# Performance work log

Hardware: AMD Instinct MI355X
Metric: run time of the kernel (lower is better)

## Reference

```python
import jax, jax.numpy as jnp
import numpy as np

F = 32          # field_size == len(feature_sizes) == mpl_dims[0]
V = 10000       # per-field vocab
D = 496         # embedding_size == comb(F, 2)
H = 1024        # mpl_dims[1]
OUT = 1         # mpl_dims[-1]
B = 16384


def setup_inputs() -> dict:
    key = jax.random.key(0)
    ks = jax.random.split(key, 8)
    xv = jax.random.normal(ks[0], (B, F), dtype=jnp.float32)
    xi = jax.random.randint(ks[1], (B, F), 0, V, dtype=jnp.int64)
    # stacked per-field embedding tables: [F, V, D]
    emb = jax.random.normal(ks[2], (F, V, D), dtype=jnp.float32) * 0.05
    W1 = jax.random.normal(ks[3], (F, H), dtype=jnp.float32) * (1.0 / np.sqrt(F))
    b1 = jax.random.normal(ks[4], (H,), dtype=jnp.float32) * 0.01
    W2 = jax.random.normal(ks[5], (H + D, OUT), dtype=jnp.float32) * (1.0 / np.sqrt(H + D))
    b2 = jax.random.normal(ks[6], (OUT,), dtype=jnp.float32) * 0.01
    return {"xv": xv, "xi": xi, "emb": emb, "W1": W1, "b1": b1, "W2": W2, "b2": b2}


def reference(xv, xi, emb, W1, b1, W2, b2):
    # Per-field embedding gather, scaled by the field value: e[b,f,:] = emb[f, xi[b,f], :] * xv[b,f]
    gathered = jax.vmap(lambda table, idx: table[idx], in_axes=(0, 1), out_axes=1)(emb, xi)  # [B, F, D]
    e = gathered * xv[:, :, None]
    # FM sum-square minus square-sum interaction -> [B, D]
    s = jnp.sum(e, axis=1)
    qi = 0.5 * (s * s - jnp.sum(e * e, axis=1))
    # MLP branch on raw values (dropout inactive at inference)
    h = jax.nn.relu(xv @ W1 + b1)  # [B, H]
    x = jnp.concatenate([qi, h], axis=1)  # [B, D + H]
    return x @ W2 + b2  # [B, OUT]
```

## Files before the change

### kernel.cpp

```cpp
#include <hip/hip_runtime.h>

constexpr int F  = 32;
constexpr int V  = 10000;
constexpr int D  = 496;
constexpr int H  = 1024;

__global__ __launch_bounds__(256, 6) void fm_kernel(
    const float* __restrict__ xv,
    const int*   __restrict__ xi,
    const float* __restrict__ emb,
    const float* __restrict__ W2,
    const float* __restrict__ b2,
    float* __restrict__ out,
    int B)
{
    const int t  = threadIdx.x;
    const int w  = t >> 6;
    const int l  = t & 63;
    const int b0 = blockIdx.x * 4;

    __shared__ float        s_xv[4][F];
    __shared__ const float* s_row[4][F];

    if (t < 128) {
        const int rr = t >> 5, f = t & 31;
        const int r  = min(b0 + rr, B - 1);
        s_xv[rr][f]  = xv[(size_t)r * F + f];
        s_row[rr][f] = emb + ((size_t)f * V + (size_t)xi[(size_t)r * F + f]) * D;
    }
    __syncthreads();

    const int   c1 = (l < 60) ? l : 59;
    const float m1 = (l < 60) ? 1.0f : 0.0f;

    float4 s0  = make_float4(0.f, 0.f, 0.f, 0.f);
    float4 ss0 = make_float4(0.f, 0.f, 0.f, 0.f);
    float4 s1  = make_float4(0.f, 0.f, 0.f, 0.f);
    float4 ss1 = make_float4(0.f, 0.f, 0.f, 0.f);

    #pragma unroll 4
    for (int f = 0; f < F; ++f) {
        const float  xf = s_xv[w][f];
        const float* p  = s_row[w][f];
        float4 v0 = *reinterpret_cast<const float4*>(p + 4 * l);
        float4 v1 = *reinterpret_cast<const float4*>(p + 256 + 4 * c1);
        v0.x *= xf; v0.y *= xf; v0.z *= xf; v0.w *= xf;
        v1.x *= xf; v1.y *= xf; v1.z *= xf; v1.w *= xf;
        s0.x  += v0.x;        s0.y  += v0.y;        s0.z  += v0.z;        s0.w  += v0.w;
        ss0.x += v0.x * v0.x; ss0.y += v0.y * v0.y; ss0.z += v0.z * v0.z; ss0.w += v0.w * v0.w;
        s1.x  += v1.x;        s1.y  += v1.y;        s1.z  += v1.z;        s1.w  += v1.w;
        ss1.x += v1.x * v1.x; ss1.y += v1.y * v1.y; ss1.z += v1.z * v1.z; ss1.w += v1.w * v1.w;
    }

    const float4 w2a = *reinterpret_cast<const float4*>(W2 + 4 * l);
    const float4 w2b = *reinterpret_cast<const float4*>(W2 + 256 + 4 * c1);

    float acc = (0.5f * (s0.x * s0.x - ss0.x)) * w2a.x
              + (0.5f * (s0.y * s0.y - ss0.y)) * w2a.y
              + (0.5f * (s0.z * s0.z - ss0.z)) * w2a.z
              + (0.5f * (s0.w * s0.w - ss0.w)) * w2a.w
        + m1 * ((0.5f * (s1.x * s1.x - ss1.x)) * w2b.x
              + (0.5f * (s1.y * s1.y - ss1.y)) * w2b.y
              + (0.5f * (s1.z * s1.z - ss1.z)) * w2b.z
              + (0.5f * (s1.w * s1.w - ss1.w)) * w2b.w);

    #pragma unroll
    for (int off = 32; off > 0; off >>= 1)
        acc += __shfl_down(acc, off, 64);
    if (l == 0 && b0 + w < B) out[b0 + w] = acc + b2[0];
}

constexpr int R  = 64;
constexpr int RC = 8;

__global__ __launch_bounds__(256, 4) void mlp_kernel(
    const float* __restrict__ xv,
    const float* __restrict__ W1,
    const float* __restrict__ b1,
    const float* __restrict__ W2,
    float* __restrict__ out,
    int B)
{
    const int t  = threadIdx.x;
    const int b0 = blockIdx.x * R;
    const int j0 = 4 * t;

    __shared__ float s_xv[F][R];
    __shared__ float s_red[RC][4];

    {
        const int r0 = t >> 3, f0 = 4 * (t & 7);
        const int rA = min(b0 + r0,      B - 1);
        const int rB = min(b0 + r0 + 32, B - 1);
        float4 v0 = *reinterpret_cast<const float4*>(xv + (size_t)rA * F + f0);
        float4 v1 = *reinterpret_cast<const float4*>(xv + (size_t)rB * F + f0);
        s_xv[f0 + 0][r0] = v0.x; s_xv[f0 + 1][r0] = v0.y;
        s_xv[f0 + 2][r0] = v0.z; s_xv[f0 + 3][r0] = v0.w;
        s_xv[f0 + 0][r0 + 32] = v1.x; s_xv[f0 + 1][r0 + 32] = v1.y;
        s_xv[f0 + 2][r0 + 32] = v1.z; s_xv[f0 + 3][r0 + 32] = v1.w;
    }
    __syncthreads();

    const float4 w2v = *reinterpret_cast<const float4*>(W2 + D + j0);
    const float4 bv  = *reinterpret_cast<const float4*>(b1 + j0);

    for (int rc = 0; rc < R; rc += RC) {
        float4 h[RC];
        #pragma unroll
        for (int r = 0; r < RC; ++r) h[r] = bv;

        #pragma unroll 4
        for (int f = 0; f < F; ++f) {
            const float4 w  = *reinterpret_cast<const float4*>(W1 + f * H + j0);
            const float4 xa = *reinterpret_cast<const float4*>(&s_xv[f][rc]);
            const float4 xb = *reinterpret_cast<const float4*>(&s_xv[f][rc + 4]);
            const float xr[RC] = {xa.x, xa.y, xa.z, xa.w, xb.x, xb.y, xb.z, xb.w};
            #pragma unroll
            for (int r = 0; r < RC; ++r) {
                h[r].x += xr[r] * w.x; h[r].y += xr[r] * w.y;
                h[r].z += xr[r] * w.z; h[r].w += xr[r] * w.w;
            }
        }

        #pragma unroll
        for (int r = 0; r < RC; ++r) {
            float p = fmaxf(h[r].x, 0.f) * w2v.x + fmaxf(h[r].y, 0.f) * w2v.y
                    + fmaxf(h[r].z, 0.f) * w2v.z + fmaxf(h[r].w, 0.f) * w2v.w;
            #pragma unroll
            for (int off = 32; off > 0; off >>= 1)
                p += __shfl_down(p, off, 64);
            if ((t & 63) == 0) s_red[r][t >> 6] = p;
        }
        __syncthreads();
        if (t < RC) {
            const int row = b0 + rc + t;
            if (row < B)
                out[row] += s_red[t][0] + s_red[t][1] + s_red[t][2] + s_red[t][3];
        }
        __syncthreads();
    }
}

extern "C" void kernel_launch(void* const* d_in, const int* in_sizes, int n_in,
                              void* d_out, int out_size, void* d_ws, size_t ws_size,
                              hipStream_t stream) {
    const float* xv  = (const float*)d_in[0];
    const int*   xi  = (const int*)d_in[1];
    const float* emb = (const float*)d_in[2];
    const float* W1  = (const float*)d_in[3];
    const float* b1  = (const float*)d_in[4];
    const float* W2  = (const float*)d_in[5];
    const float* b2  = (const float*)d_in[6];
    float* out = (float*)d_out;

    const int B = in_sizes[0] / F;

    fm_kernel<<<(B + 3) / 4, 256, 0, stream>>>(xv, xi, emb, W2, b2, out, B);
    mlp_kernel<<<(B + R - 1) / R, 256, 0, stream>>>(xv, W1, b1, W2, out, B);
}
```

Baseline: 899.3 us.

## Merge FM and MLP kernels into one heterogeneous launch with combine pass

Fuses the FM gather kernel and the MLP kernel into a single grid, where the first nMLP blocks run the MLP branch and the rest run the FM branch. Partial results go to workspace, and a small combine kernel sums them with the bias. The aim is to let the compute-heavy MLP blocks overlap with the memory-bound gather blocks instead of running them one after the other. The fused kernel uses the MLP's lower occupancy bound (256,4) for the FM path too, and the extra combine launch adds a little overhead.

New measurement: 838.6 us. 6.8% less time.

```diff
diff --git a/kernel.cpp b/kernel.cpp
--- a/kernel.cpp
+++ b/kernel.cpp
@@ -4,141 +4,142 @@
 constexpr int V  = 10000;
 constexpr int D  = 496;
 constexpr int H  = 1024;
+constexpr int RM = 64;
+constexpr int RC = 8;
 
-__global__ __launch_bounds__(256, 6) void fm_kernel(
+__global__ __launch_bounds__(256, 4) void deepqi_hetero(
     const float* __restrict__ xv,
     const int*   __restrict__ xi,
     const float* __restrict__ emb,
-    const float* __restrict__ W2,
-    const float* __restrict__ b2,
-    float* __restrict__ out,
-    int B)
-{
-    const int t  = threadIdx.x;
-    const int w  = t >> 6;
-    const int l  = t & 63;
-    const int b0 = blockIdx.x * 4;
-
-    __shared__ float        s_xv[4][F];
-    __shared__ const float* s_row[4][F];
-
-    if (t < 128) {
-        const int rr = t >> 5, f = t & 31;
-        const int r  = min(b0 + rr, B - 1);
-        s_xv[rr][f]  = xv[(size_t)r * F + f];
-        s_row[rr][f] = emb + ((size_t)f * V + (size_t)xi[(size_t)r * F + f]) * D;
-    }
-    __syncthreads();
-
-    const int   c1 = (l < 60) ? l : 59;
-    const float m1 = (l < 60) ? 1.0f : 0.0f;
-
-    float4 s0  = make_float4(0.f, 0.f, 0.f, 0.f);
-    float4 ss0 = make_float4(0.f, 0.f, 0.f, 0.f);
-    float4 s1  = make_float4(0.f, 0.f, 0.f, 0.f);
-    float4 ss1 = make_float4(0.f, 0.f, 0.f, 0.f);
-
-    #pragma unroll 4
-    for (int f = 0; f < F; ++f) {
-        const float  xf = s_xv[w][f];
-        const float* p  = s_row[w][f];
-        float4 v0 = *reinterpret_cast<const float4*>(p + 4 * l);
-        float4 v1 = *reinterpret_cast<const float4*>(p + 256 + 4 * c1);
-        v0.x *= xf; v0.y *= xf; v0.z *= xf; v0.w *= xf;
-        v1.x *= xf; v1.y *= xf; v1.z *= xf; v1.w *= xf;
-        s0.x  += v0.x;        s0.y  += v0.y;        s0.z  += v0.z;        s0.w  += v0.w;
-        ss0.x += v0.x * v0.x; ss0.y += v0.y * v0.y; ss0.z += v0.z * v0.z; ss0.w += v0.w * v0.w;
-        s1.x  += v1.x;        s1.y  += v1.y;        s1.z  += v1.z;        s1.w  += v1.w;
-        ss1.x += v1.x * v1.x; ss1.y += v1.y * v1.y; ss1.z += v1.z * v1.z; ss1.w += v1.w * v1.w;
-    }
-
-    const float4 w2a = *reinterpret_cast<const float4*>(W2 + 4 * l);
-    const float4 w2b = *reinterpret_cast<const float4*>(W2 + 256 + 4 * c1);
-
-    float acc = (0.5f * (s0.x * s0.x - ss0.x)) * w2a.x
-              + (0.5f * (s0.y * s0.y - ss0.y)) * w2a.y
-              + (0.5f * (s0.z * s0.z - ss0.z)) * w2a.z
-              + (0.5f * (s0.w * s0.w - ss0.w)) * w2a.w
-        + m1 * ((0.5f * (s1.x * s1.x - ss1.x)) * w2b.x
-              + (0.5f * (s1.y * s1.y - ss1.y)) * w2b.y
-              + (0.5f * (s1.z * s1.z - ss1.z)) * w2b.z
-              + (0.5f * (s1.w * s1.w - ss1.w)) * w2b.w);
-
-    #pragma unroll
-    for (int off = 32; off > 0; off >>= 1)
-        acc += __shfl_down(acc, off, 64);
-    if (l == 0 && b0 + w < B) out[b0 + w] = acc + b2[0];
-}
-
-constexpr int R  = 64;
-constexpr int RC = 8;
-
-__global__ __launch_bounds__(256, 4) void mlp_kernel(
-    const float* __restrict__ xv,
     const float* __restrict__ W1,
     const float* __restrict__ b1,
     const float* __restrict__ W2,
-    float* __restrict__ out,
-    int B)
+    float* __restrict__ ws,
+    int B, int nMLP)
 {
-    const int t  = threadIdx.x;
-    const int b0 = blockIdx.x * R;
-    const int j0 = 4 * t;
+    const int t = threadIdx.x;
 
-    __shared__ float s_xv[F][R];
-    __shared__ float s_red[RC][4];
+    if ((int)blockIdx.x < nMLP) {
+        const int b0 = blockIdx.x * RM;
+        const int j0 = 4 * t;
 
-    {
-        const int r0 = t >> 3, f0 = 4 * (t & 7);
-        const int rA = min(b0 + r0,      B - 1);
-        const int rB = min(b0 + r0 + 32, B - 1);
-        float4 v0 = *reinterpret_cast<const float4*>(xv + (size_t)rA * F + f0);
-        float4 v1 = *reinterpret_cast<const float4*>(xv + (size_t)rB * F + f0);
-        s_xv[f0 + 0][r0] = v0.x; s_xv[f0 + 1][r0] = v0.y;
-        s_xv[f0 + 2][r0] = v0.z; s_xv[f0 + 3][r0] = v0.w;
-        s_xv[f0 + 0][r0 + 32] = v1.x; s_xv[f0 + 1][r0 + 32] = v1.y;
-        s_xv[f0 + 2][r0 + 32] = v1.z; s_xv[f0 + 3][r0 + 32] = v1.w;
-    }
-    __syncthreads();
+        __shared__ float s_xv[F][RM];
+        __shared__ float s_red[RC][4];
 
-    const float4 w2v = *reinterpret_cast<const float4*>(W2 + D + j0);
-    const float4 bv  = *reinterpret_cast<const float4*>(b1 + j0);
+        {
+            const int r0 = t >> 3, f0 = 4 * (t & 7);
+            const int rA = min(b0 + r0,      B - 1);
+            const int rB = min(b0 + r0 + 32, B - 1);
+            float4 v0 = *reinterpret_cast<const float4*>(xv + (size_t)rA * F + f0);
+            float4 v1 = *reinterpret_cast<const float4*>(xv + (size_t)rB * F + f0);
+            s_xv[f0 + 0][r0] = v0.x; s_xv[f0 + 1][r0] = v0.y;
+            s_xv[f0 + 2][r0] = v0.z; s_xv[f0 + 3][r0] = v0.w;
+            s_xv[f0 + 0][r0 + 32] = v1.x; s_xv[f0 + 1][r0 + 32] = v1.y;
+            s_xv[f0 + 2][r0 + 32] = v1.z; s_xv[f0 + 3][r0 + 32] = v1.w;
+        }
+        __syncthreads();
 
-    for (int rc = 0; rc < R; rc += RC) {
-        float4 h[RC];
-        #pragma unroll
-        for (int r = 0; r < RC; ++r) h[r] = bv;
+        const float4 w2v = *reinterpret_cast<const float4*>(W2 + D + j0);
+        const float4 bv  = *reinterpret_cast<const float4*>(b1 + j0);
+
+        for (int rc = 0; rc < RM; rc += RC) {
+            float4 h[RC];
+            #pragma unroll
+            for (int r = 0; r < RC; ++r) h[r] = bv;
+
+            #pragma unroll 4
+            for (int f = 0; f < F; ++f) {
+                const float4 w  = *reinterpret_cast<const float4*>(W1 + f * H + j0);
+                const float4 xa = *reinterpret_cast<const float4*>(&s_xv[f][rc]);
+                const float4 xb = *reinterpret_cast<const float4*>(&s_xv[f][rc + 4]);
+                const float xr[RC] = {xa.x, xa.y, xa.z, xa.w, xb.x, xb.y, xb.z, xb.w};
+                #pragma unroll
+                for (int r = 0; r < RC; ++r) {
+                    h[r].x += xr[r] * w.x; h[r].y += xr[r] * w.y;
+                    h[r].z += xr[r] * w.z; h[r].w += xr[r] * w.w;
+                }
+            }
+
+            #pragma unroll
+            for (int r = 0; r < RC; ++r) {
+                float p = fmaxf(h[r].x, 0.f) * w2v.x + fmaxf(h[r].y, 0.f) * w2v.y
+                        + fmaxf(h[r].z, 0.f) * w2v.z + fmaxf(h[r].w, 0.f) * w2v.w;
+                #pragma unroll
+                for (int off = 32; off > 0; off >>= 1)
+                    p += __shfl_down(p, off, 64);
+                if ((t & 63) == 0) s_red[r][t >> 6] = p;
+            }
+            __syncthreads();
+            if (t < RC) {
+                const int row = b0 + rc + t;
+                if (row < B)
+                    ws[(size_t)B + row] = s_red[t][0] + s_red[t][1] + s_red[t][2] + s_red[t][3];
+            }
+            __syncthreads();
+        }
+    } else {
+        const int w  = t >> 6;
+        const int l  = t & 63;
+        const int b0 = ((int)blockIdx.x - nMLP) * 4;
+
+        __shared__ float        s_xv2[4][F];
+        __shared__ const float* s_row[4][F];
+
+        if (t < 128) {
+            const int rr = t >> 5, f = t & 31;
+            const int r  = min(b0 + rr, B - 1);
+            s_xv2[rr][f] = xv[(size_t)r * F + f];
+            s_row[rr][f] = emb + ((size_t)f * V + (size_t)xi[(size_t)r * F + f]) * D;
+        }
+        __syncthreads();
+
+        const int   c1 = (l < 60) ? l : 59;
+        const float m1 = (l < 60) ? 1.0f : 0.0f;
+
+        float4 s0  = make_float4(0.f, 0.f, 0.f, 0.f);
+        float4 ss0 = make_float4(0.f, 0.f, 0.f, 0.f);
+        float4 s1  = make_float4(0.f, 0.f, 0.f, 0.f);
+        float4 ss1 = make_float4(0.f, 0.f, 0.f, 0.f);
 
         #pragma unroll 4
         for (int f = 0; f < F; ++f) {
-            const float4 w  = *reinterpret_cast<const float4*>(W1 + f * H + j0);
-            const float4 xa = *reinterpret_cast<const float4*>(&s_xv[f][rc]);
-            const float4 xb = *reinterpret_cast<const float4*>(&s_xv[f][rc + 4]);
-            const float xr[RC] = {xa.x, xa.y, xa.z, xa.w, xb.x, xb.y, xb.z, xb.w};
-            #pragma unroll
-            for (int r = 0; r < RC; ++r) {
-                h[r].x += xr[r] * w.x; h[r].y += xr[r] * w.y;
-                h[r].z += xr[r] * w.z; h[r].w += xr[r] * w.w;
-            }
+            const float  xf = s_xv2[w][f];
+            const float* p  = s_row[w][f];
+            float4 v0 = *reinterpret_cast<const float4*>(p + 4 * l);
+            float4 v1 = *reinterpret_cast<const float4*>(p + 256 + 4 * c1);
+            v0.x *= xf; v0.y *= xf; v0.z *= xf; v0.w *= xf;
+            v1.x *= xf; v1.y *= xf; v1.z *= xf; v1.w *= xf;
+            s0.x  += v0.x;        s0.y  += v0.y;        s0.z  += v0.z;        s0.w  += v0.w;
+            ss0.x += v0.x * v0.x; ss0.y += v0.y * v0.y; ss0.z += v0.z * v0.z; ss0.w += v0.w * v0.w;
+            s1.x  += v1.x;        s1.y  += v1.y;        s1.z  += v1.z;        s1.w  += v1.w;
+            ss1.x += v1.x * v1.x; ss1.y += v1.y * v1.y; ss1.z += v1.z * v1.z; ss1.w += v1.w * v1.w;
         }
 
+        const float4 w2a = *reinterpret_cast<const float4*>(W2 + 4 * l);
+        const float4 w2b = *reinterpret_cast<const float4*>(W2 + 256 + 4 * c1);
+
+        float acc = (0.5f * (s0.x * s0.x - ss0.x)) * w2a.x
+                  + (0.5f * (s0.y * s0.y - ss0.y)) * w2a.y
+                  + (0.5f * (s0.z * s0.z - ss0.z)) * w2a.z
+                  + (0.5f * (s0.w * s0.w - ss0.w)) * w2a.w
+            + m1 * ((0.5f * (s1.x * s1.x - ss1.x)) * w2b.x
+                  + (0.5f * (s1.y * s1.y - ss1.y)) * w2b.y
+                  + (0.5f * (s1.z * s1.z - ss1.z)) * w2b.z
+                  + (0.5f * (s1.w * s1.w - ss1.w)) * w2b.w);
+
         #pragma unroll
-        for (int r = 0; r < RC; ++r) {
-            float p = fmaxf(h[r].x, 0.f) * w2v.x + fmaxf(h[r].y, 0.f) * w2v.y
-                    + fmaxf(h[r].z, 0.f) * w2v.z + fmaxf(h[r].w, 0.f) * w2v.w;
-            #pragma unroll
-            for (int off = 32; off > 0; off >>= 1)
-                p += __shfl_down(p, off, 64);
-            if ((t & 63) == 0) s_red[r][t >> 6] = p;
-        }
-        __syncthreads();
-        if (t < RC) {
-            const int row = b0 + rc + t;
-            if (row < B)
-                out[row] += s_red[t][0] + s_red[t][1] + s_red[t][2] + s_red[t][3];
-        }
-        __syncthreads();
+        for (int off = 32; off > 0; off >>= 1)
+            acc += __shfl_down(acc, off, 64);
+        if (l == 0 && b0 + w < B) ws[b0 + w] = acc;
     }
+}
+
+__global__ __launch_bounds__(256) void combine_kernel(
+    const float* __restrict__ ws, const float* __restrict__ b2,
+    float* __restrict__ out, int B)
+{
+    const int i = blockIdx.x * 256 + threadIdx.x;
+    if (i < B) out[i] = ws[i] + ws[(size_t)B + i] + b2[0];
 }
 
 extern "C" void kernel_launch(void* const* d_in, const int* in_sizes, int n_in,
@@ -152,9 +153,12 @@
     const float* W2  = (const float*)d_in[5];
     const float* b2  = (const float*)d_in[6];
     float* out = (float*)d_out;
+    float* ws  = (float*)d_ws;
 
-    const int B = in_sizes[0] / F;
+    const int B    = in_sizes[0] / F;
+    const int nMLP = (B + RM - 1) / RM;
+    const int nFM  = (B + 3) / 4;
 
-    fm_kernel<<<(B + 3) / 4, 256, 0, stream>>>(xv, xi, emb, W2, b2, out, B);
-    mlp_kernel<<<(B + R - 1) / R, 256, 0, stream>>>(xv, W1, b1, W2, out, B);
+    deepqi_hetero<<<nMLP + nFM, 256, 0, stream>>>(xv, xi, emb, W1, b1, W2, ws, B, nMLP);
+    combine_kernel<<<(B + 255) / 256, 256, 0, stream>>>(ws, b2, out, B);
 }
```
